# Performance work log

Measured on AMD Instinct MI355X. Metric: run time of the kernel, lower is better.

Reference implementation:

```python
import jax, jax.numpy as jnp
import numpy as np

EPS = 1e-7
N_NODES = 100000

# --- Lorentz model (c = 1), working at the origin o = (1, 0, ..., 0) ---

def expmap0(v_spatial):
    """Exp map at origin: tangent spatial part [N, d] -> hyperboloid point [N, d+1]."""
    nrm = jnp.sqrt(jnp.maximum(jnp.sum(v_spatial * v_spatial, axis=-1, keepdims=True), EPS))
    x0 = jnp.cosh(nrm)
    xs = jnp.sinh(nrm) / nrm * v_spatial
    return jnp.concatenate([x0, xs], axis=-1)


def logmap0(x):
    """Log map at origin: point [N, d+1] -> tangent spatial part [N, d]."""
    x0 = jnp.maximum(x[..., :1], 1.0 + EPS)
    xs = x[..., 1:]
    nrm = jnp.sqrt(jnp.maximum(jnp.sum(xs * xs, axis=-1, keepdims=True), EPS))
    return jnp.arccosh(x0) / nrm * xs


def sigmoid_nonlin(x):
    # log map -> sigmoid in tangent space -> exp map (c_in = c_out = 1)
    return expmap0(jax.nn.sigmoid(logmap0(x)))


def hgcn_layer(x, edge_index, W, b):
    """HGCN conv: tangent-space linear + mean aggregation over edges + exp map."""
    t = logmap0(x)                      # [N, d_in]
    h = t @ W + b                       # [N, d_out]
    src, dst = edge_index[0], edge_index[1]
    msg = h[src]                        # [E, d_out] gather
    agg = jax.ops.segment_sum(msg, dst, num_segments=N_NODES)
    deg = jax.ops.segment_sum(jnp.ones((edge_index.shape[1],), h.dtype), dst,
                              num_segments=N_NODES)
    agg = agg / jnp.maximum(deg, 1.0)[:, None]
    return expmap0(agg)


def setup_inputs() -> dict:
    key = jax.random.key(0)
    ks = jax.random.split(key, 10)
    d_in, h1, h2, h_mlp, d_out = 64, 64, 64, 128, 40
    return {
        "features": jax.random.normal(ks[0], (N_NODES, d_in), jnp.float32),
        "edge_index": jax.random.randint(ks[1], (2, 1600000), 0, N_NODES, jnp.int64),
        "W1": jax.random.normal(ks[2], (d_in, h1), jnp.float32) * 0.05,
        "b1": jnp.zeros((h1,), jnp.float32),
        "W2": jax.random.normal(ks[3], (h1, h2), jnp.float32) * 0.05,
        "b2": jnp.zeros((h2,), jnp.float32),
        "W3": jax.random.normal(ks[4], (h2, h_mlp), jnp.float32) * 0.05,
        "b3": jnp.zeros((h_mlp,), jnp.float32),
        "W4": jax.random.normal(ks[5], (h_mlp, d_out), jnp.float32) * 0.05,
        "b4": jnp.zeros((d_out,), jnp.float32),
    }


def reference(features, edge_index, W1, b1, W2, b2, W3, b3, W4, b4):
    # lift Euclidean features to the hyperboloid (pad time coord, exp map)
    x = expmap0(features)                       # [N, d_in+1]
    x = hgcn_layer(x, edge_index, W1, b1)
    x = sigmoid_nonlin(x)
    x = hgcn_layer(x, edge_index, W2, b2)
    x = sigmoid_nonlin(x)
    t = logmap0(x)                              # [N, h2] (spatial part, drops time coord)
    # MLP head (dropout inactive at eval)
    h = jax.nn.relu(t @ W3 + b3)
    return h @ W4 + b4
```

## Files before the change

kernel.cpp:

```cpp
#include <hip/hip_runtime.h>


constexpr int CSHIFT = 9;
constexpr int CNODES = 1 << CSHIFT;
constexpr int EPB    = 4096;
constexpr int PTHR   = 512;
constexpr int EPT    = EPB / PTHR;
constexpr int CAP    = 16384;

constexpr int W1F_OFF = 0;
constexpr int W2F_OFF = 4096;
constexpr int W3F_OFF = 8192;
constexpr int W4F_OFF = 16384;
constexpr int WIMG_TOT = 22528;

typedef __attribute__((ext_vector_type(8))) short short8;
typedef __attribute__((ext_vector_type(4))) float floatx4;

__device__ __forceinline__ float sigmoidf(float x) {
    return 1.0f / (1.0f + __expf(-x));
}
__device__ __forceinline__ unsigned short f2bf(float f) {
    unsigned int u = __float_as_uint(f);
    u = (u + 0x7FFFu + ((u >> 16) & 1u)) >> 16;
    return (unsigned short)u;
}

__global__ __launch_bounds__(512) void part_prep_k(
    const int* __restrict__ src, const int* __restrict__ dst,
    int* __restrict__ ccur, int* __restrict__ arena, int E, int NBUCK, int gP,
    const float* __restrict__ feat, unsigned short* __restrict__ featbf,
    const float* __restrict__ W1, const float* __restrict__ W2,
    const float* __restrict__ W3, const float* __restrict__ W4,
    unsigned short* __restrict__ img, int n8)
{
    __shared__ int  hist[256];
    __shared__ int  exoff[256];
    __shared__ int  lcur[256];
    __shared__ int  gbase[256];
    __shared__ int  wsum[4];
    __shared__ int  stage[EPB];
    __shared__ unsigned char stageB[EPB];

    const int tid = threadIdx.x;

    if ((int)blockIdx.x >= gP) {
        int i = ((int)blockIdx.x - gP) * PTHR + tid;
        if (i < n8) {
            const float4* p = (const float4*)feat + (size_t)i * 2;
            float4 a = p[0], b = p[1];
            uint4 o;
            o.x = (unsigned)f2bf(a.x) | ((unsigned)f2bf(a.y) << 16);
            o.y = (unsigned)f2bf(a.z) | ((unsigned)f2bf(a.w) << 16);
            o.z = (unsigned)f2bf(b.x) | ((unsigned)f2bf(b.y) << 16);
            o.w = (unsigned)f2bf(b.z) | ((unsigned)f2bf(b.w) << 16);
            ((uint4*)featbf)[i] = o;
            return;
        }
        int t = i - n8;
        if (t >= WIMG_TOT) return;
        float v = 0.f;
        int s = t;
        if (s < W2F_OFF) {
            int j = s & 7, m = (s >> 3) & 15, q = (s >> 7) & 3, kk = (s >> 9) & 1, c = s >> 10;
            v = W1[(kk * 32 + q * 8 + j) * 64 + c * 16 + m];
        } else if (s < W3F_OFF) {
            s -= W2F_OFF;
            int j = s & 7, m = (s >> 3) & 15, q = (s >> 7) & 3, kk = (s >> 9) & 1, c = s >> 10;
            v = W2[(kk * 32 + q * 8 + j) * 64 + c * 16 + m];
        } else if (s < W4F_OFF) {
            s -= W3F_OFF;
            int j = s & 7, m = (s >> 3) & 15, q = (s >> 7) & 3, kk = (s >> 9) & 1, c = s >> 10;
            v = W3[(kk * 32 + q * 8 + j) * 128 + c * 16 + m];
        } else {
            s -= W4F_OFF;
            int j = s & 7, m = (s >> 3) & 15, q = (s >> 7) & 3, kk = (s >> 9) & 3, c = s >> 11;
            int n = c * 16 + m;
            if (n < 40) v = W4[(kk * 32 + q * 8 + j) * 40 + n];
        }
        img[t] = f2bf(v);
        return;
    }

    const int e0  = blockIdx.x * EPB;
    const int ec  = min(EPB, E - e0);
    const int lane = tid & 63, wid = tid >> 6;

    int pk[EPT], bk[EPT];
    if (tid < 256) hist[tid] = 0;
    __syncthreads();
    #pragma unroll
    for (int j = 0; j < EPT; j++) {
        int idx = tid + j * PTHR;
        if (idx < ec) {
            int s = src[e0 + idx];
            int d = dst[e0 + idx];
            bk[j] = d >> CSHIFT;
            pk[j] = s | ((d & (CNODES - 1)) << 17);
            atomicAdd(&hist[bk[j]], 1);
        } else bk[j] = -1;
    }
    __syncthreads();
    int h = 0, v = 0;
    if (tid < 256) {
        h = hist[tid];
        v = h;
        #pragma unroll
        for (int d = 1; d < 64; d <<= 1) {
            int t = __shfl_up(v, d);
            if (lane >= d) v += t;
        }
        if (lane == 63) wsum[wid] = v;
    }
    __syncthreads();
    if (tid == 0) {
        int s = 0;
        #pragma unroll
        for (int k = 0; k < 4; k++) { int t = wsum[k]; wsum[k] = s; s += t; }
    }
    __syncthreads();
    if (tid < 256) {
        int ex = wsum[wid] + v - h;
        int gb = 0;
        if (tid < NBUCK && h > 0) gb = atomicAdd(ccur + tid, h);
        exoff[tid] = ex;
        lcur[tid]  = ex;
        gbase[tid] = gb;
    }
    __syncthreads();
    #pragma unroll
    for (int j = 0; j < EPT; j++) {
        if (bk[j] >= 0) {
            int l = atomicAdd(&lcur[bk[j]], 1);
            stage[l]  = pk[j];
            stageB[l] = (unsigned char)bk[j];
        }
    }
    __syncthreads();
    for (int i = tid; i < ec; i += PTHR) {
        int b = stageB[i];
        arena[(size_t)b * CAP + gbase[b] + (i - exoff[b])] = stage[i];
    }
}

__global__ __launch_bounds__(1024) void csr_fine(const int* __restrict__ arena,
                                                 const int* __restrict__ ccur,
                                                 int* __restrict__ off,
                                                 int* __restrict__ ssrc,
                                                 int N, int E, int NBUCK) {
    __shared__ int part[256];
    __shared__ int cnt[CNODES];
    __shared__ int cur[CNODES];
    __shared__ int wpre[8];
    const int b = blockIdx.x;
    const int node0 = b << CSHIFT;
    const int tid = threadIdx.x;
    const int lane = tid & 63, wid = tid >> 6;

    if (tid < 256) part[tid] = (tid < NBUCK) ? ccur[tid] : 0;
    __syncthreads();
    for (int d = 1; d < 256; d <<= 1) {
        int v = 0;
        if (tid < 256 && tid >= d) v = part[tid - d];
        __syncthreads();
        if (tid < 256 && tid >= d) part[tid] += v;
        __syncthreads();
    }
    const int cbeg = (b > 0) ? part[b - 1] : 0;
    const int ec   = min(ccur[b], CAP);
    if (b == 0 && tid == 0) off[N] = E;

    if (tid < CNODES) cnt[tid] = 0;
    __syncthreads();
    const int* pe = arena + (size_t)b * CAP;
    for (int i = tid; i < ec; i += 1024)
        atomicAdd(&cnt[(pe[i] >> 17) & (CNODES - 1)], 1);
    __syncthreads();

    int c = (tid < CNODES) ? cnt[tid] : 0;
    int v = c;
    #pragma unroll
    for (int d = 1; d < 64; d <<= 1) {
        int t = __shfl_up(v, d);
        if (lane >= d) v += t;
    }
    if (tid < CNODES && lane == 63) wpre[wid] = v;
    __syncthreads();
    if (tid == 0) {
        int s = 0;
        #pragma unroll
        for (int k = 0; k < CNODES / 64; k++) { int t = wpre[k]; wpre[k] = s; s += t; }
    }
    __syncthreads();
    if (tid < CNODES) {
        int ex = wpre[wid] + v - c;
        cur[tid] = ex;
        int node = node0 + tid;
        if (node < N) off[node] = cbeg + ex;
    }
    __syncthreads();
    for (int i = tid; i < ec; i += 1024) {
        int p = pe[i];
        int pos = cbeg + atomicAdd(&cur[(p >> 17) & (CNODES - 1)], 1);
        ssrc[pos] = p & 0x1FFFF;
    }
}

#define ACC8(v)                                    \
    acc[0] += __uint_as_float((v).x << 16);        \
    acc[1] += __uint_as_float((v).x & 0xFFFF0000u);\
    acc[2] += __uint_as_float((v).y << 16);        \
    acc[3] += __uint_as_float((v).y & 0xFFFF0000u);\
    acc[4] += __uint_as_float((v).z << 16);        \
    acc[5] += __uint_as_float((v).z & 0xFFFF0000u);\
    acc[6] += __uint_as_float((v).w << 16);        \
    acc[7] += __uint_as_float((v).w & 0xFFFF0000u);

__device__ __forceinline__ void gather_tile_wave(
    const unsigned short* __restrict__ h, const int* __restrict__ off,
    const int* __restrict__ ssrc, unsigned short* Agg, int rowB, int N,
    int w, int lane)
{
    #pragma unroll
    for (int pass = 0; pass < 2; pass++) {
        int rl = w * 16 + pass * 8 + (lane >> 3);
        int g  = rowB + rl;
        int q  = (lane & 7) * 8;
        uint4 p = make_uint4(0u, 0u, 0u, 0u);
        if (g < N) {
            int beg = off[g], end = off[g + 1];
            float acc[8] = {0.f, 0.f, 0.f, 0.f, 0.f, 0.f, 0.f, 0.f};
            int i = beg;
            for (; i + 16 <= end; i += 16) {
                int s0 = ssrc[i],      s1 = ssrc[i + 1];
                int s2 = ssrc[i + 2],  s3 = ssrc[i + 3];
                int s4 = ssrc[i + 4],  s5 = ssrc[i + 5];
                int s6 = ssrc[i + 6],  s7 = ssrc[i + 7];
                int s8 = ssrc[i + 8],  s9 = ssrc[i + 9];
                int sa = ssrc[i + 10], sb = ssrc[i + 11];
                int sc = ssrc[i + 12], sd = ssrc[i + 13];
                int se = ssrc[i + 14], sf = ssrc[i + 15];
                uint4 v0 = *(const uint4*)(h + (size_t)s0 * 64 + q);
                uint4 v1 = *(const uint4*)(h + (size_t)s1 * 64 + q);
                uint4 v2 = *(const uint4*)(h + (size_t)s2 * 64 + q);
                uint4 v3 = *(const uint4*)(h + (size_t)s3 * 64 + q);
                uint4 v4 = *(const uint4*)(h + (size_t)s4 * 64 + q);
                uint4 v5 = *(const uint4*)(h + (size_t)s5 * 64 + q);
                uint4 v6 = *(const uint4*)(h + (size_t)s6 * 64 + q);
                uint4 v7 = *(const uint4*)(h + (size_t)s7 * 64 + q);
                uint4 v8 = *(const uint4*)(h + (size_t)s8 * 64 + q);
                uint4 v9 = *(const uint4*)(h + (size_t)s9 * 64 + q);
                uint4 va = *(const uint4*)(h + (size_t)sa * 64 + q);
                uint4 vb = *(const uint4*)(h + (size_t)sb * 64 + q);
                uint4 vc = *(const uint4*)(h + (size_t)sc * 64 + q);
                uint4 vd = *(const uint4*)(h + (size_t)sd * 64 + q);
                uint4 ve = *(const uint4*)(h + (size_t)se * 64 + q);
                uint4 vf = *(const uint4*)(h + (size_t)sf * 64 + q);
                ACC8(v0); ACC8(v1); ACC8(v2); ACC8(v3);
                ACC8(v4); ACC8(v5); ACC8(v6); ACC8(v7);
                ACC8(v8); ACC8(v9); ACC8(va); ACC8(vb);
                ACC8(vc); ACC8(vd); ACC8(ve); ACC8(vf);
            }
            for (; i + 4 <= end; i += 4) {
                int s0 = ssrc[i],     s1 = ssrc[i + 1];
                int s2 = ssrc[i + 2], s3 = ssrc[i + 3];
                uint4 v0 = *(const uint4*)(h + (size_t)s0 * 64 + q);
                uint4 v1 = *(const uint4*)(h + (size_t)s1 * 64 + q);
                uint4 v2 = *(const uint4*)(h + (size_t)s2 * 64 + q);
                uint4 v3 = *(const uint4*)(h + (size_t)s3 * 64 + q);
                ACC8(v0); ACC8(v1); ACC8(v2); ACC8(v3);
            }
            for (; i < end; i++) {
                uint4 v = *(const uint4*)(h + (size_t)ssrc[i] * 64 + q);
                ACC8(v);
            }
            float inv = __builtin_amdgcn_rcpf((float)max(end - beg, 1));
            p.x = (unsigned)f2bf(acc[0]*inv) | ((unsigned)f2bf(acc[1]*inv) << 16);
            p.y = (unsigned)f2bf(acc[2]*inv) | ((unsigned)f2bf(acc[3]*inv) << 16);
            p.z = (unsigned)f2bf(acc[4]*inv) | ((unsigned)f2bf(acc[5]*inv) << 16);
            p.w = (unsigned)f2bf(acc[6]*inv) | ((unsigned)f2bf(acc[7]*inv) << 16);
        }
        *(uint4*)(Agg + rl * 72 + q) = p;
    }
}

__global__ __launch_bounds__(128) void aggemm1_k(
    const unsigned short* __restrict__ featbf, const int* __restrict__ off,
    const int* __restrict__ ssrc, const unsigned short* __restrict__ img,
    const float* __restrict__ bias, unsigned short* __restrict__ t1, int N)
{
    __shared__ alignas(16) unsigned short Agg[32 * 72];

    const int tid = threadIdx.x;
    const int rowB = blockIdx.x * 32;
    const int w = tid >> 6, lane = tid & 63;
    const int m = lane & 15, quad = lane >> 4;
    const int row0 = rowB + w * 16;

    gather_tile_wave(featbf, off, ssrc, Agg, rowB, N, w, lane);

    const short8* Wf = (const short8*)(img + W1F_OFF);
    floatx4 acc[4];
    #pragma unroll
    for (int c = 0; c < 4; c++) acc[c] = (floatx4){0.f, 0.f, 0.f, 0.f};
    #pragma unroll
    for (int kk = 0; kk < 2; kk++) {
        short8 a = *(const short8*)(Agg + (w * 16 + m) * 72 + kk * 32 + quad * 8);
        #pragma unroll
        for (int c = 0; c < 4; c++) {
            short8 b = Wf[((c * 2 + kk) * 4 + quad) * 16 + m];
            acc[c] = __builtin_amdgcn_mfma_f32_16x16x32_bf16(a, b, acc[c], 0, 0, 0);
        }
    }
    bool dzr[4];
    int rows[4];
    #pragma unroll
    for (int r = 0; r < 4; r++) {
        rows[r] = row0 + quad * 4 + r;
        dzr[r] = (rows[r] < N) ? (off[rows[r] + 1] == off[rows[r]]) : false;
    }
    #pragma unroll
    for (int c = 0; c < 4; c++) {
        int col = c * 16 + m;
        float bv = bias[col];
        #pragma unroll
        for (int r = 0; r < 4; r++) {
            if (rows[r] < N) {
                float v = dzr[r] ? 0.5f : sigmoidf(acc[c][r] + bv);
                t1[(size_t)rows[r] * 64 + col] = f2bf(v);
            }
        }
    }
}

__global__ __launch_bounds__(128) void aggep3_k(
    const unsigned short* __restrict__ t1, const int* __restrict__ off,
    const int* __restrict__ ssrc, const unsigned short* __restrict__ img,
    const float* __restrict__ b2, const float* __restrict__ b3,
    const float* __restrict__ b4, float* __restrict__ out, int N)
{
    __shared__ alignas(16) unsigned short SM[4608];
    unsigned short* T2  = SM;
    unsigned short* Agg = SM + 2304;
    unsigned short* H3h = SM + 2304;

    const int tid = threadIdx.x;
    const int rowB = blockIdx.x * 32;
    const int w = tid >> 6, lane = tid & 63;
    const int m = lane & 15, quad = lane >> 4;
    const int row0 = rowB + w * 16;

    gather_tile_wave(t1, off, ssrc, Agg, rowB, N, w, lane);

    {
        const short8* Wf = (const short8*)(img + W2F_OFF);
        floatx4 acc[4];
        #pragma unroll
        for (int c = 0; c < 4; c++) acc[c] = (floatx4){0.f, 0.f, 0.f, 0.f};
        #pragma unroll
        for (int kk = 0; kk < 2; kk++) {
            short8 a = *(const short8*)(Agg + (w * 16 + m) * 72 + kk * 32 + quad * 8);
            #pragma unroll
            for (int c = 0; c < 4; c++) {
                short8 b = Wf[((c * 2 + kk) * 4 + quad) * 16 + m];
                acc[c] = __builtin_amdgcn_mfma_f32_16x16x32_bf16(a, b, acc[c], 0, 0, 0);
            }
        }
        bool dzr[4];
        #pragma unroll
        for (int r = 0; r < 4; r++) {
            int row = row0 + quad * 4 + r;
            dzr[r] = (row < N) ? (off[row + 1] == off[row]) : false;
        }
        #pragma unroll
        for (int c = 0; c < 4; c++) {
            int col = c * 16 + m;
            float bv = b2[col];
            #pragma unroll
            for (int r = 0; r < 4; r++) {
                int rl = w * 16 + quad * 4 + r;
                float v = dzr[r] ? 0.5f : sigmoidf(acc[c][r] + bv);
                T2[rl * 72 + col] = f2bf(v);
            }
        }
    }

    floatx4 acc2[3];
    #pragma unroll
    for (int c = 0; c < 3; c++) acc2[c] = (floatx4){0.f, 0.f, 0.f, 0.f};
    const short8* Wf3 = (const short8*)(img + W3F_OFF);
    const short8* Wf4 = (const short8*)(img + W4F_OFF);

    #pragma unroll
    for (int half = 0; half < 2; half++) {
        floatx4 acc[4];
        #pragma unroll
        for (int c = 0; c < 4; c++) acc[c] = (floatx4){0.f, 0.f, 0.f, 0.f};
        #pragma unroll
        for (int kk = 0; kk < 2; kk++) {
            short8 a = *(const short8*)(T2 + (w * 16 + m) * 72 + kk * 32 + quad * 8);
            #pragma unroll
            for (int c = 0; c < 4; c++) {
                short8 b = Wf3[(((half * 4 + c) * 2 + kk) * 4 + quad) * 16 + m];
                acc[c] = __builtin_amdgcn_mfma_f32_16x16x32_bf16(a, b, acc[c], 0, 0, 0);
            }
        }
        #pragma unroll
        for (int c = 0; c < 4; c++) {
            int col = c * 16 + m;
            float bv = b3[half * 64 + col];
            #pragma unroll
            for (int r = 0; r < 4; r++) {
                int rl = w * 16 + quad * 4 + r;
                H3h[rl * 72 + col] = f2bf(fmaxf(acc[c][r] + bv, 0.f));
            }
        }
        #pragma unroll
        for (int kk2 = 0; kk2 < 2; kk2++) {
            short8 a = *(const short8*)(H3h + (w * 16 + m) * 72 + kk2 * 32 + quad * 8);
            #pragma unroll
            for (int c = 0; c < 3; c++) {
                short8 b = Wf4[((c * 4 + half * 2 + kk2) * 4 + quad) * 16 + m];
                acc2[c] = __builtin_amdgcn_mfma_f32_16x16x32_bf16(a, b, acc2[c], 0, 0, 0);
            }
        }
    }

    #pragma unroll
    for (int c = 0; c < 3; c++) {
        int col = c * 16 + m;
        if (col < 40) {
            float bv = b4[col];
            #pragma unroll
            for (int r = 0; r < 4; r++) {
                int row = row0 + quad * 4 + r;
                if (row < N) out[(size_t)row * 40 + col] = acc2[c][r] + bv;
            }
        }
    }
}

extern "C" void kernel_launch(void* const* d_in, const int* in_sizes, int n_in,
                              void* d_out, int out_size, void* d_ws, size_t ws_size,
                              hipStream_t stream)
{
    const float* feat = (const float*)d_in[0];
    const int*   eidx = (const int*)d_in[1];
    const float* W1 = (const float*)d_in[2];
    const float* b1 = (const float*)d_in[3];
    const float* W2 = (const float*)d_in[4];
    const float* b2 = (const float*)d_in[5];
    const float* W3 = (const float*)d_in[6];
    const float* b3 = (const float*)d_in[7];
    const float* W4 = (const float*)d_in[8];
    const float* b4 = (const float*)d_in[9];

    const int N = in_sizes[0] / 64;
    const int E = in_sizes[1] / 2;
    const int* src = eidx;
    const int* dst = eidx + E;

    const int NBUCK = (N + CNODES - 1) / CNODES;

    unsigned short* featbf = (unsigned short*)d_ws;
    unsigned short* t1     = featbf + (size_t)N * 64;
    unsigned short* img    = t1     + (size_t)N * 64;
    int*   off   = (int*)(img + WIMG_TOT);
    int*   ccur  = off + (N + 1);
    int*   ssrc  = ccur + NBUCK;
    int*   arena = ssrc + E;
    float* out   = (float*)d_out;

    hipMemsetAsync(ccur, 0, (size_t)NBUCK * sizeof(int), stream);

    const int gP  = (E + EPB - 1) / EPB;
    const int g32 = (N + 31) / 32;
    const int n8  = N * 64 / 8;
    const int gPC = (n8 + WIMG_TOT + PTHR - 1) / PTHR;

    part_prep_k<<<gP + gPC, dim3(PTHR), 0, stream>>>(src, dst, ccur, arena, E,
                                                     NBUCK, gP, feat, featbf,
                                                     W1, W2, W3, W4, img, n8);
    csr_fine<<<NBUCK, dim3(1024), 0, stream>>>(arena, ccur, off, ssrc, N, E, NBUCK);

    aggemm1_k<<<g32, dim3(128), 0, stream>>>(featbf, off, ssrc, img, b1, t1, N);
    aggep3_k<<<g32, dim3(128), 0, stream>>>(t1, off, ssrc, img, b2, b3, b4, out, N);
}
```

Before: 225.6 us.

## Use single-wave 16-row blocks and interleave two rows' neighbor gathers

Each fused aggregate+GEMM kernel now runs one 64-lane wave per block over 16 rows instead of two waves over 32 rows, with half the shared memory. In the gather, each lane group processes its two rows together, issuing loads for both in 8-wide chunks, so two independent load streams are in flight. The 16-wide unroll becomes 8-wide per row. This aims to raise memory-level parallelism and shrink per-block tail imbalance. The cost is twice as many blocks and different register pressure under launch_bounds(64,4).

```diff
diff --git a/kernel.cpp b/kernel.cpp
--- a/kernel.cpp
+++ b/kernel.cpp
@@ -206,98 +206,106 @@
     }
 }
 
-#define ACC8(v)                                    \
-    acc[0] += __uint_as_float((v).x << 16);        \
-    acc[1] += __uint_as_float((v).x & 0xFFFF0000u);\
-    acc[2] += __uint_as_float((v).y << 16);        \
-    acc[3] += __uint_as_float((v).y & 0xFFFF0000u);\
-    acc[4] += __uint_as_float((v).z << 16);        \
-    acc[5] += __uint_as_float((v).z & 0xFFFF0000u);\
-    acc[6] += __uint_as_float((v).w << 16);        \
-    acc[7] += __uint_as_float((v).w & 0xFFFF0000u);
-
-__device__ __forceinline__ void gather_tile_wave(
+#define ACC8T(A, v)                                 \
+    A[0] += __uint_as_float((v).x << 16);           \
+    A[1] += __uint_as_float((v).x & 0xFFFF0000u);   \
+    A[2] += __uint_as_float((v).y << 16);           \
+    A[3] += __uint_as_float((v).y & 0xFFFF0000u);   \
+    A[4] += __uint_as_float((v).z << 16);           \
+    A[5] += __uint_as_float((v).z & 0xFFFF0000u);   \
+    A[6] += __uint_as_float((v).w << 16);           \
+    A[7] += __uint_as_float((v).w & 0xFFFF0000u);
+
+#define LD8(P, base, i)                                             \
+    {                                                               \
+        int s0 = ssrc[i],     s1 = ssrc[(i)+1];                     \
+        int s2 = ssrc[(i)+2], s3 = ssrc[(i)+3];                     \
+        int s4 = ssrc[(i)+4], s5 = ssrc[(i)+5];                     \
+        int s6 = ssrc[(i)+6], s7 = ssrc[(i)+7];                     \
+        uint4 v0 = *(const uint4*)(h + (size_t)s0 * 64 + q);        \
+        uint4 v1 = *(const uint4*)(h + (size_t)s1 * 64 + q);        \
+        uint4 v2 = *(const uint4*)(h + (size_t)s2 * 64 + q);        \
+        uint4 v3 = *(const uint4*)(h + (size_t)s3 * 64 + q);        \
+        uint4 v4 = *(const uint4*)(h + (size_t)s4 * 64 + q);        \
+        uint4 v5 = *(const uint4*)(h + (size_t)s5 * 64 + q);        \
+        uint4 v6 = *(const uint4*)(h + (size_t)s6 * 64 + q);        \
+        uint4 v7 = *(const uint4*)(h + (size_t)s7 * 64 + q);        \
+        ACC8T(P, v0); ACC8T(P, v1); ACC8T(P, v2); ACC8T(P, v3);     \
+        ACC8T(P, v4); ACC8T(P, v5); ACC8T(P, v6); ACC8T(P, v7);     \
+    }
+
+__device__ __forceinline__ void gather_rows16(
     const unsigned short* __restrict__ h, const int* __restrict__ off,
     const int* __restrict__ ssrc, unsigned short* Agg, int rowB, int N,
-    int w, int lane)
+    int lane)
 {
-    #pragma unroll
-    for (int pass = 0; pass < 2; pass++) {
-        int rl = w * 16 + pass * 8 + (lane >> 3);
-        int g  = rowB + rl;
-        int q  = (lane & 7) * 8;
-        uint4 p = make_uint4(0u, 0u, 0u, 0u);
-        if (g < N) {
-            int beg = off[g], end = off[g + 1];
-            float acc[8] = {0.f, 0.f, 0.f, 0.f, 0.f, 0.f, 0.f, 0.f};
-            int i = beg;
-            for (; i + 16 <= end; i += 16) {
-                int s0 = ssrc[i],      s1 = ssrc[i + 1];
-                int s2 = ssrc[i + 2],  s3 = ssrc[i + 3];
-                int s4 = ssrc[i + 4],  s5 = ssrc[i + 5];
-                int s6 = ssrc[i + 6],  s7 = ssrc[i + 7];
-                int s8 = ssrc[i + 8],  s9 = ssrc[i + 9];
-                int sa = ssrc[i + 10], sb = ssrc[i + 11];
-                int sc = ssrc[i + 12], sd = ssrc[i + 13];
-                int se = ssrc[i + 14], sf = ssrc[i + 15];
-                uint4 v0 = *(const uint4*)(h + (size_t)s0 * 64 + q);
-                uint4 v1 = *(const uint4*)(h + (size_t)s1 * 64 + q);
-                uint4 v2 = *(const uint4*)(h + (size_t)s2 * 64 + q);
-                uint4 v3 = *(const uint4*)(h + (size_t)s3 * 64 + q);
-                uint4 v4 = *(const uint4*)(h + (size_t)s4 * 64 + q);
-                uint4 v5 = *(const uint4*)(h + (size_t)s5 * 64 + q);
-                uint4 v6 = *(const uint4*)(h + (size_t)s6 * 64 + q);
-                uint4 v7 = *(const uint4*)(h + (size_t)s7 * 64 + q);
-                uint4 v8 = *(const uint4*)(h + (size_t)s8 * 64 + q);
-                uint4 v9 = *(const uint4*)(h + (size_t)s9 * 64 + q);
-                uint4 va = *(const uint4*)(h + (size_t)sa * 64 + q);
-                uint4 vb = *(const uint4*)(h + (size_t)sb * 64 + q);
-                uint4 vc = *(const uint4*)(h + (size_t)sc * 64 + q);
-                uint4 vd = *(const uint4*)(h + (size_t)sd * 64 + q);
-                uint4 ve = *(const uint4*)(h + (size_t)se * 64 + q);
-                uint4 vf = *(const uint4*)(h + (size_t)sf * 64 + q);
-                ACC8(v0); ACC8(v1); ACC8(v2); ACC8(v3);
-                ACC8(v4); ACC8(v5); ACC8(v6); ACC8(v7);
-                ACC8(v8); ACC8(v9); ACC8(va); ACC8(vb);
-                ACC8(vc); ACC8(vd); ACC8(ve); ACC8(vf);
-            }
-            for (; i + 4 <= end; i += 4) {
-                int s0 = ssrc[i],     s1 = ssrc[i + 1];
-                int s2 = ssrc[i + 2], s3 = ssrc[i + 3];
-                uint4 v0 = *(const uint4*)(h + (size_t)s0 * 64 + q);
-                uint4 v1 = *(const uint4*)(h + (size_t)s1 * 64 + q);
-                uint4 v2 = *(const uint4*)(h + (size_t)s2 * 64 + q);
-                uint4 v3 = *(const uint4*)(h + (size_t)s3 * 64 + q);
-                ACC8(v0); ACC8(v1); ACC8(v2); ACC8(v3);
-            }
-            for (; i < end; i++) {
-                uint4 v = *(const uint4*)(h + (size_t)ssrc[i] * 64 + q);
-                ACC8(v);
-            }
-            float inv = __builtin_amdgcn_rcpf((float)max(end - beg, 1));
-            p.x = (unsigned)f2bf(acc[0]*inv) | ((unsigned)f2bf(acc[1]*inv) << 16);
-            p.y = (unsigned)f2bf(acc[2]*inv) | ((unsigned)f2bf(acc[3]*inv) << 16);
-            p.z = (unsigned)f2bf(acc[4]*inv) | ((unsigned)f2bf(acc[5]*inv) << 16);
-            p.w = (unsigned)f2bf(acc[6]*inv) | ((unsigned)f2bf(acc[7]*inv) << 16);
-        }
-        *(uint4*)(Agg + rl * 72 + q) = p;
-    }
-}
-
-__global__ __launch_bounds__(128) void aggemm1_k(
+    const int grp = lane >> 3;
+    const int q   = (lane & 7) * 8;
+    const int rl0 = grp, rl1 = grp + 8;
+    const int g0 = rowB + rl0, g1 = rowB + rl1;
+
+    float acc0[8] = {0.f, 0.f, 0.f, 0.f, 0.f, 0.f, 0.f, 0.f};
+    float acc1[8] = {0.f, 0.f, 0.f, 0.f, 0.f, 0.f, 0.f, 0.f};
+    int i0 = 0, e0 = 0, i1 = 0, e1 = 0;
+    if (g0 < N) { i0 = off[g0]; e0 = off[g0 + 1]; }
+    if (g1 < N) { i1 = off[g1]; e1 = off[g1 + 1]; }
+    const int d0 = e0 - i0, d1 = e1 - i1;
+
+    while (i0 + 8 <= e0 && i1 + 8 <= e1) {
+        LD8(acc0, h, i0);
+        LD8(acc1, h, i1);
+        i0 += 8; i1 += 8;
+    }
+    for (; i0 + 8 <= e0; i0 += 8) LD8(acc0, h, i0);
+    for (; i0 + 2 <= e0; i0 += 2) {
+        int s0 = ssrc[i0], s1 = ssrc[i0 + 1];
+        uint4 v0 = *(const uint4*)(h + (size_t)s0 * 64 + q);
+        uint4 v1 = *(const uint4*)(h + (size_t)s1 * 64 + q);
+        ACC8T(acc0, v0); ACC8T(acc0, v1);
+    }
+    for (; i0 < e0; i0++) {
+        uint4 v = *(const uint4*)(h + (size_t)ssrc[i0] * 64 + q);
+        ACC8T(acc0, v);
+    }
+    for (; i1 + 8 <= e1; i1 += 8) LD8(acc1, h, i1);
+    for (; i1 + 2 <= e1; i1 += 2) {
+        int s0 = ssrc[i1], s1 = ssrc[i1 + 1];
+        uint4 v0 = *(const uint4*)(h + (size_t)s0 * 64 + q);
+        uint4 v1 = *(const uint4*)(h + (size_t)s1 * 64 + q);
+        ACC8T(acc1, v0); ACC8T(acc1, v1);
+    }
+    for (; i1 < e1; i1++) {
+        uint4 v = *(const uint4*)(h + (size_t)ssrc[i1] * 64 + q);
+        ACC8T(acc1, v);
+    }
+
+    float inv0 = __builtin_amdgcn_rcpf((float)max(d0, 1));
+    float inv1 = __builtin_amdgcn_rcpf((float)max(d1, 1));
+    uint4 p0, p1;
+    p0.x = (unsigned)f2bf(acc0[0]*inv0) | ((unsigned)f2bf(acc0[1]*inv0) << 16);
+    p0.y = (unsigned)f2bf(acc0[2]*inv0) | ((unsigned)f2bf(acc0[3]*inv0) << 16);
+    p0.z = (unsigned)f2bf(acc0[4]*inv0) | ((unsigned)f2bf(acc0[5]*inv0) << 16);
+    p0.w = (unsigned)f2bf(acc0[6]*inv0) | ((unsigned)f2bf(acc0[7]*inv0) << 16);
+    p1.x = (unsigned)f2bf(acc1[0]*inv1) | ((unsigned)f2bf(acc1[1]*inv1) << 16);
+    p1.y = (unsigned)f2bf(acc1[2]*inv1) | ((unsigned)f2bf(acc1[3]*inv1) << 16);
+    p1.z = (unsigned)f2bf(acc1[4]*inv1) | ((unsigned)f2bf(acc1[5]*inv1) << 16);
+    p1.w = (unsigned)f2bf(acc1[6]*inv1) | ((unsigned)f2bf(acc1[7]*inv1) << 16);
+    *(uint4*)(Agg + rl0 * 72 + q) = p0;
+    *(uint4*)(Agg + rl1 * 72 + q) = p1;
+}
+
+__global__ __launch_bounds__(64, 4) void aggemm1_k(
     const unsigned short* __restrict__ featbf, const int* __restrict__ off,
     const int* __restrict__ ssrc, const unsigned short* __restrict__ img,
     const float* __restrict__ bias, unsigned short* __restrict__ t1, int N)
 {
-    __shared__ alignas(16) unsigned short Agg[32 * 72];
-
-    const int tid = threadIdx.x;
-    const int rowB = blockIdx.x * 32;
-    const int w = tid >> 6, lane = tid & 63;
+    __shared__ alignas(16) unsigned short Agg[16 * 72];
+
+    const int lane = threadIdx.x;
+    const int rowB = blockIdx.x * 16;
     const int m = lane & 15, quad = lane >> 4;
-    const int row0 = rowB + w * 16;
-
-    gather_tile_wave(featbf, off, ssrc, Agg, rowB, N, w, lane);
+
+    gather_rows16(featbf, off, ssrc, Agg, rowB, N, lane);
 
     const short8* Wf = (const short8*)(img + W1F_OFF);
     floatx4 acc[4];
@@ -305,7 +313,7 @@
     for (int c = 0; c < 4; c++) acc[c] = (floatx4){0.f, 0.f, 0.f, 0.f};
     #pragma unroll
     for (int kk = 0; kk < 2; kk++) {
-        short8 a = *(const short8*)(Agg + (w * 16 + m) * 72 + kk * 32 + quad * 8);
+        short8 a = *(const short8*)(Agg + m * 72 + kk * 32 + quad * 8);
         #pragma unroll
         for (int c = 0; c < 4; c++) {
             short8 b = Wf[((c * 2 + kk) * 4 + quad) * 16 + m];
@@ -316,7 +324,7 @@
     int rows[4];
     #pragma unroll
     for (int r = 0; r < 4; r++) {
-        rows[r] = row0 + quad * 4 + r;
+        rows[r] = rowB + quad * 4 + r;
         dzr[r] = (rows[r] < N) ? (off[rows[r] + 1] == off[rows[r]]) : false;
     }
     #pragma unroll
@@ -333,24 +341,22 @@
     }
 }
 
-__global__ __launch_bounds__(128) void aggep3_k(
+__global__ __launch_bounds__(64, 4) void aggep3_k(
     const unsigned short* __restrict__ t1, const int* __restrict__ off,
     const int* __restrict__ ssrc, const unsigned short* __restrict__ img,
     const float* __restrict__ b2, const float* __restrict__ b3,
     const float* __restrict__ b4, float* __restrict__ out, int N)
 {
-    __shared__ alignas(16) unsigned short SM[4608];
+    __shared__ alignas(16) unsigned short SM[2304];
     unsigned short* T2  = SM;
-    unsigned short* Agg = SM + 2304;
-    unsigned short* H3h = SM + 2304;
-
-    const int tid = threadIdx.x;
-    const int rowB = blockIdx.x * 32;
-    const int w = tid >> 6, lane = tid & 63;
+    unsigned short* Agg = SM + 1152;
+    unsigned short* H3h = SM + 1152;
+
+    const int lane = threadIdx.x;
+    const int rowB = blockIdx.x * 16;
     const int m = lane & 15, quad = lane >> 4;
-    const int row0 = rowB + w * 16;
-
-    gather_tile_wave(t1, off, ssrc, Agg, rowB, N, w, lane);
+
+    gather_rows16(t1, off, ssrc, Agg, rowB, N, lane);
 
     {
         const short8* Wf = (const short8*)(img + W2F_OFF);
@@ -359,7 +365,7 @@
         for (int c = 0; c < 4; c++) acc[c] = (floatx4){0.f, 0.f, 0.f, 0.f};
         #pragma unroll
         for (int kk = 0; kk < 2; kk++) {
-            short8 a = *(const short8*)(Agg + (w * 16 + m) * 72 + kk * 32 + quad * 8);
+            short8 a = *(const short8*)(Agg + m * 72 + kk * 32 + quad * 8);
             #pragma unroll
             for (int c = 0; c < 4; c++) {
                 short8 b = Wf[((c * 2 + kk) * 4 + quad) * 16 + m];
@@ -369,7 +375,7 @@
         bool dzr[4];
         #pragma unroll
         for (int r = 0; r < 4; r++) {
-            int row = row0 + quad * 4 + r;
+            int row = rowB + quad * 4 + r;
             dzr[r] = (row < N) ? (off[row + 1] == off[row]) : false;
         }
         #pragma unroll
@@ -378,7 +384,7 @@
             float bv = b2[col];
             #pragma unroll
             for (int r = 0; r < 4; r++) {
-                int rl = w * 16 + quad * 4 + r;
+                int rl = quad * 4 + r;
                 float v = dzr[r] ? 0.5f : sigmoidf(acc[c][r] + bv);
                 T2[rl * 72 + col] = f2bf(v);
             }
@@ -398,7 +404,7 @@
         for (int c = 0; c < 4; c++) acc[c] = (floatx4){0.f, 0.f, 0.f, 0.f};
         #pragma unroll
         for (int kk = 0; kk < 2; kk++) {
-            short8 a = *(const short8*)(T2 + (w * 16 + m) * 72 + kk * 32 + quad * 8);
+            short8 a = *(const short8*)(T2 + m * 72 + kk * 32 + quad * 8);
             #pragma unroll
             for (int c = 0; c < 4; c++) {
                 short8 b = Wf3[(((half * 4 + c) * 2 + kk) * 4 + quad) * 16 + m];
@@ -411,13 +417,13 @@
             float bv = b3[half * 64 + col];
             #pragma unroll
             for (int r = 0; r < 4; r++) {
-                int rl = w * 16 + quad * 4 + r;
+                int rl = quad * 4 + r;
                 H3h[rl * 72 + col] = f2bf(fmaxf(acc[c][r] + bv, 0.f));
             }
         }
         #pragma unroll
         for (int kk2 = 0; kk2 < 2; kk2++) {
-            short8 a = *(const short8*)(H3h + (w * 16 + m) * 72 + kk2 * 32 + quad * 8);
+            short8 a = *(const short8*)(H3h + m * 72 + kk2 * 32 + quad * 8);
             #pragma unroll
             for (int c = 0; c < 3; c++) {
                 short8 b = Wf4[((c * 4 + half * 2 + kk2) * 4 + quad) * 16 + m];
@@ -433,7 +439,7 @@
             float bv = b4[col];
             #pragma unroll
             for (int r = 0; r < 4; r++) {
-                int row = row0 + quad * 4 + r;
+                int row = rowB + quad * 4 + r;
                 if (row < N) out[(size_t)row * 40 + col] = acc2[c][r] + bv;
             }
         }
@@ -474,7 +480,7 @@
     hipMemsetAsync(ccur, 0, (size_t)NBUCK * sizeof(int), stream);
 
     const int gP  = (E + EPB - 1) / EPB;
-    const int g32 = (N + 31) / 32;
+    const int g16 = (N + 15) / 16;
     const int n8  = N * 64 / 8;
     const int gPC = (n8 + WIMG_TOT + PTHR - 1) / PTHR;
 
@@ -483,6 +489,6 @@
                                                      W1, W2, W3, W4, img, n8);
     csr_fine<<<NBUCK, dim3(1024), 0, stream>>>(arena, ccur, off, ssrc, N, E, NBUCK);
 
-    aggemm1_k<<<g32, dim3(128), 0, stream>>>(featbf, off, ssrc, img, b1, t1, N);
-    aggep3_k<<<g32, dim3(128), 0, stream>>>(t1, off, ssrc, img, b2, b3, b4, out, N);
-}
+    aggemm1_k<<<g16, dim3(64), 0, stream>>>(featbf, off, ssrc, img, b1, t1, N);
+    aggep3_k<<<g16, dim3(64), 0, stream>>>(t1, off, ssrc, img, b2, b3, b4, out, N);
+}
```

New measurement: 220.4 us. -2.3%, faster.

## Sort CSR neighbors by coarse source chunk and shrink gather unroll

Applied to the files above, without the earlier changes.

The CSR build now counts and scatters edges into bins keyed by destination node and a coarse source-range chunk (8 chunks). Each node's neighbor list is therefore roughly ordered by source index, so concurrent gathers across rows touch similar regions of the feature table and should reuse L2/MALL better. The prefix scan now covers 4096 bins with four per thread. The gather inner loop drops from 16-way to 8-way unroll with a 2-way tail, trading memory-level parallelism for lower register pressure.

```diff
diff --git a/kernel.cpp b/kernel.cpp
--- a/kernel.cpp
+++ b/kernel.cpp
@@ -7,6 +7,9 @@
 constexpr int PTHR   = 512;
 constexpr int EPT    = EPB / PTHR;
 constexpr int CAP    = 16384;
+constexpr int SSH    = 14;
+constexpr int NCH    = 8;
+constexpr int NBIN   = CNODES * NCH;
 
 constexpr int W1F_OFF = 0;
 constexpr int W2F_OFF = 4096;
@@ -149,9 +152,9 @@
                                                  int* __restrict__ ssrc,
                                                  int N, int E, int NBUCK) {
     __shared__ int part[256];
-    __shared__ int cnt[CNODES];
-    __shared__ int cur[CNODES];
-    __shared__ int wpre[8];
+    __shared__ int cnt[NBIN];
+    __shared__ int cur[NBIN];
+    __shared__ int wpre[16];
     const int b = blockIdx.x;
     const int node0 = b << CSHIFT;
     const int tid = threadIdx.x;
@@ -170,38 +173,57 @@
     const int ec   = min(ccur[b], CAP);
     if (b == 0 && tid == 0) off[N] = E;
 
-    if (tid < CNODES) cnt[tid] = 0;
+    #pragma unroll
+    for (int k = 0; k < NBIN / 1024; k++) cnt[tid + k * 1024] = 0;
     __syncthreads();
     const int* pe = arena + (size_t)b * CAP;
-    for (int i = tid; i < ec; i += 1024)
-        atomicAdd(&cnt[(pe[i] >> 17) & (CNODES - 1)], 1);
-    __syncthreads();
-
-    int c = (tid < CNODES) ? cnt[tid] : 0;
-    int v = c;
+    for (int i = tid; i < ec; i += 1024) {
+        int p = pe[i];
+        int key = (((p >> 17) & (CNODES - 1)) << 3) | ((p & 0x1FFFF) >> SSH);
+        atomicAdd(&cnt[key], 1);
+    }
+    __syncthreads();
+
+    const int t4 = tid * 4;
+    int s0 = cnt[t4], s1 = cnt[t4 + 1], s2 = cnt[t4 + 2], s3 = cnt[t4 + 3];
+    int l1 = s0, l2 = s0 + s1, l3 = s0 + s1 + s2;
+    int tsum = l3 + s3;
+    int v = tsum;
     #pragma unroll
     for (int d = 1; d < 64; d <<= 1) {
         int t = __shfl_up(v, d);
         if (lane >= d) v += t;
     }
-    if (tid < CNODES && lane == 63) wpre[wid] = v;
+    if (lane == 63) wpre[wid] = v;
     __syncthreads();
     if (tid == 0) {
         int s = 0;
         #pragma unroll
-        for (int k = 0; k < CNODES / 64; k++) { int t = wpre[k]; wpre[k] = s; s += t; }
-    }
-    __syncthreads();
-    if (tid < CNODES) {
-        int ex = wpre[wid] + v - c;
-        cur[tid] = ex;
-        int node = node0 + tid;
-        if (node < N) off[node] = cbeg + ex;
+        for (int k = 0; k < 16; k++) { int t = wpre[k]; wpre[k] = s; s += t; }
+    }
+    __syncthreads();
+    const int ex0 = wpre[wid] + v - tsum;
+    cur[t4]     = ex0;
+    cur[t4 + 1] = ex0 + l1;
+    cur[t4 + 2] = ex0 + l2;
+    cur[t4 + 3] = ex0 + l3;
+    {
+        int bin = t4;
+        if ((bin & 7) == 0) {
+            int node = node0 + (bin >> 3);
+            if (node < N) off[node] = cbeg + ex0;
+        }
+        bin = t4 + 4;
+        if ((bin & 7) == 0) {
+            int node = node0 + (bin >> 3);
+            if (node < N) off[node] = cbeg + ex0 + l3 + s3 - s3 + 0;
+        }
     }
     __syncthreads();
     for (int i = tid; i < ec; i += 1024) {
         int p = pe[i];
-        int pos = cbeg + atomicAdd(&cur[(p >> 17) & (CNODES - 1)], 1);
+        int key = (((p >> 17) & (CNODES - 1)) << 3) | ((p & 0x1FFFF) >> SSH);
+        int pos = cbeg + atomicAdd(&cur[key], 1);
         ssrc[pos] = p & 0x1FFFF;
     }
 }
@@ -231,44 +253,22 @@
             int beg = off[g], end = off[g + 1];
             float acc[8] = {0.f, 0.f, 0.f, 0.f, 0.f, 0.f, 0.f, 0.f};
             int i = beg;
-            for (; i + 16 <= end; i += 16) {
-                int s0 = ssrc[i],      s1 = ssrc[i + 1];
-                int s2 = ssrc[i + 2],  s3 = ssrc[i + 3];
-                int s4 = ssrc[i + 4],  s5 = ssrc[i + 5];
-                int s6 = ssrc[i + 6],  s7 = ssrc[i + 7];
-                int s8 = ssrc[i + 8],  s9 = ssrc[i + 9];
-                int sa = ssrc[i + 10], sb = ssrc[i + 11];
-                int sc = ssrc[i + 12], sd = ssrc[i + 13];
-                int se = ssrc[i + 14], sf = ssrc[i + 15];
-                uint4 v0 = *(const uint4*)(h + (size_t)s0 * 64 + q);
-                uint4 v1 = *(const uint4*)(h + (size_t)s1 * 64 + q);
-                uint4 v2 = *(const uint4*)(h + (size_t)s2 * 64 + q);
-                uint4 v3 = *(const uint4*)(h + (size_t)s3 * 64 + q);
-                uint4 v4 = *(const uint4*)(h + (size_t)s4 * 64 + q);
-                uint4 v5 = *(const uint4*)(h + (size_t)s5 * 64 + q);
-                uint4 v6 = *(const uint4*)(h + (size_t)s6 * 64 + q);
-                uint4 v7 = *(const uint4*)(h + (size_t)s7 * 64 + q);
-                uint4 v8 = *(const uint4*)(h + (size_t)s8 * 64 + q);
-                uint4 v9 = *(const uint4*)(h + (size_t)s9 * 64 + q);
-                uint4 va = *(const uint4*)(h + (size_t)sa * 64 + q);
-                uint4 vb = *(const uint4*)(h + (size_t)sb * 64 + q);
-                uint4 vc = *(const uint4*)(h + (size_t)sc * 64 + q);
-                uint4 vd = *(const uint4*)(h + (size_t)sd * 64 + q);
-                uint4 ve = *(const uint4*)(h + (size_t)se * 64 + q);
-                uint4 vf = *(const uint4*)(h + (size_t)sf * 64 + q);
+            for (; i + 8 <= end; i += 8) {
+                uint4 v0 = *(const uint4*)(h + (size_t)ssrc[i]     * 64 + q);
+                uint4 v1 = *(const uint4*)(h + (size_t)ssrc[i + 1] * 64 + q);
+                uint4 v2 = *(const uint4*)(h + (size_t)ssrc[i + 2] * 64 + q);
+                uint4 v3 = *(const uint4*)(h + (size_t)ssrc[i + 3] * 64 + q);
+                uint4 v4 = *(const uint4*)(h + (size_t)ssrc[i + 4] * 64 + q);
+                uint4 v5 = *(const uint4*)(h + (size_t)ssrc[i + 5] * 64 + q);
+                uint4 v6 = *(const uint4*)(h + (size_t)ssrc[i + 6] * 64 + q);
+                uint4 v7 = *(const uint4*)(h + (size_t)ssrc[i + 7] * 64 + q);
                 ACC8(v0); ACC8(v1); ACC8(v2); ACC8(v3);
                 ACC8(v4); ACC8(v5); ACC8(v6); ACC8(v7);
-                ACC8(v8); ACC8(v9); ACC8(va); ACC8(vb);
-                ACC8(vc); ACC8(vd); ACC8(ve); ACC8(vf);
-            }
-            for (; i + 4 <= end; i += 4) {
-                int s0 = ssrc[i],     s1 = ssrc[i + 1];
-                int s2 = ssrc[i + 2], s3 = ssrc[i + 3];
-                uint4 v0 = *(const uint4*)(h + (size_t)s0 * 64 + q);
-                uint4 v1 = *(const uint4*)(h + (size_t)s1 * 64 + q);
-                uint4 v2 = *(const uint4*)(h + (size_t)s2 * 64 + q);
-                uint4 v3 = *(const uint4*)(h + (size_t)s3 * 64 + q);
-                ACC8(v0); ACC8(v1); ACC8(v2); ACC8(v3);
+            }
+            for (; i + 2 <= end; i += 2) {
+                uint4 v0 = *(const uint4*)(h + (size_t)ssrc[i]     * 64 + q);
+                uint4 v1 = *(const uint4*)(h + (size_t)ssrc[i + 1] * 64 + q);
+                ACC8(v0); ACC8(v1);
             }
             for (; i < end; i++) {
                 uint4 v = *(const uint4*)(h + (size_t)ssrc[i] * 64 + q);
```

After: 214.5 us. 5.0% less time.
